# Optimization experiments

Measured on AMD Instinct MI355X. Metric: run time of the kernel, lower is better.

The kernel has to match this reference:

```python
import jax, jax.numpy as jnp
import numpy as np

B, N, C, K = 8, 49104, 90, 1000  # batch, anchors, classes, pre-NMS top-k cap
NEG = -1e9


def _decode(reg, anc):
    # anchors ltrb -> cxcywh, apply reg, back to ltrb (matches decode_boxes)
    l, t, r, b = anc[..., 0], anc[..., 1], anc[..., 2], anc[..., 3]
    w_a, h_a = r - l, b - t
    cx_a, cy_a = l + w_a / 2, t + h_a / 2
    cx = cx_a + reg[..., 0] * w_a
    cy = cy_a + reg[..., 1] * h_a
    w = w_a * jnp.exp(reg[..., 2])
    h = h_a * jnp.exp(reg[..., 3])
    left, top = cx - w / 2, cy - h / 2
    return jnp.stack([left, top, left + w, top + h], -1)


def _iou(boxes):  # [K,4] -> [K,K]
    area = (boxes[:, 2] - boxes[:, 0]) * (boxes[:, 3] - boxes[:, 1])
    lt = jnp.maximum(boxes[:, None, :2], boxes[None, :, :2])
    rb = jnp.minimum(boxes[:, None, 2:], boxes[None, :, 2:])
    wh = jnp.clip(rb - lt, 0.0)
    inter = wh[..., 0] * wh[..., 1]
    return inter / (area[:, None] + area[None, :] - inter + 1e-9)


def _per_image(cls, reg, anchors, size, size_ori, score_thresh, nms_thresh):
    scores = jnp.max(cls, axis=-1)                       # [N]
    labels = jnp.argmax(cls, axis=-1).astype(jnp.int32)  # [N]
    valid = scores >= score_thresh
    boxes = _decode(reg, anchors)                        # [N,4] ltrb
    H = size[0].astype(jnp.float32)
    W = size[1].astype(jnp.float32)
    x = jnp.clip(boxes[..., 0::2], 0.0, W - 1.0)
    y = jnp.clip(boxes[..., 1::2], 0.0, H - 1.0)
    boxes = jnp.stack([x[..., 0], y[..., 0], x[..., 1], y[..., 1]], -1)
    # fixed-size substitute for nonzero(): take top-K by masked score
    ms = jnp.where(valid, scores, NEG)
    top_s, idx = jax.lax.top_k(ms, K)
    b, l, v = boxes[idx], labels[idx], valid[idx]        # [K,4],[K],[K]
    # batched_nms trick: offset boxes per class so classes never overlap
    off = l.astype(jnp.float32) * (jnp.maximum(W, H) + 1.0)
    iou = _iou(b + off[:, None])                         # [K,K]
    ar = jnp.arange(K)
    def body(i, supp):
        keep_i = v[i] & jnp.logical_not(supp[i])
        return supp | (keep_i & (iou[i] > nms_thresh) & (ar > i))
    supp = jax.lax.fori_loop(0, K, body, jnp.zeros((K,), bool))
    keep = v & jnp.logical_not(supp)
    scale = size_ori[0].astype(jnp.float32) / H
    b = b * scale
    out5 = jnp.concatenate(
        [jnp.where(keep[:, None], b, 0.0), jnp.where(keep, top_s, 0.0)[:, None]], -1)
    return out5, jnp.where(keep, l, -1), keep


def setup_inputs() -> dict:
    key = jax.random.key(0)
    k1, k2, k3, k4, k5, k6 = jax.random.split(key, 6)
    classifications = jax.random.uniform(k1, (B, N, C), dtype=jnp.float32)
    regressions = jax.random.normal(k2, (B, N, 4), dtype=jnp.float32) * 0.1
    cx = jax.random.uniform(k3, (N,), minval=0.0, maxval=512.0)
    cy = jax.random.uniform(k4, (N,), minval=0.0, maxval=512.0)
    w = jax.random.uniform(k5, (N,), minval=16.0, maxval=256.0)
    h = jax.random.uniform(k6, (N,), minval=16.0, maxval=256.0)
    anchors = jnp.stack([cx - w / 2, cy - h / 2, cx + w / 2, cy + h / 2], -1)
    return {
        'classifications': classifications,
        'regressions': regressions,
        'anchors': anchors,
        'image_sizes': jnp.full((B, 2), 512, dtype=jnp.int32),
        'image_sizes_ori': jnp.full((B, 2), 768, dtype=jnp.int32),
        'score_thresh': jnp.float32(0.999),
        'nms_thresh': jnp.float32(0.5),
    }


def reference(classifications, regressions, anchors, image_sizes, image_sizes_ori, score_thresh, nms_thresh):
    out5, labels, keep = jax.vmap(
        _per_image, in_axes=(0, 0, None, 0, 0, None, None))(
        classifications, regressions, anchors, image_sizes, image_sizes_ori,
        score_thresh, nms_thresh)
    return out5, labels, keep
```

## Files before the change

kernel.cpp:

```cpp
#include <hip/hip_runtime.h>
#include <stdint.h>

#define NB 8
#define NN 49104
#define NNP 49152
#define NC 90
#define NK 1000
#define CAP2 8192
#define SEG 1024
#define CHUNK 6144
#define NB2 4352
#define NB2P 5120

typedef unsigned long long u64;

__global__ void k_score(const float* __restrict__ cls,
                        const float* __restrict__ thr_p,
                        u64* __restrict__ keys) {
  __shared__ float lds[64 * NC];
  int b = blockIdx.y;
  int t0 = blockIdx.x * 64;
  int acnt = NN - t0; if (acnt > 64) acnt = 64;
  const float4* src = (const float4*)(cls + ((size_t)b * NN + t0) * NC);
  float4* dst = (float4*)lds;
  int elems4 = acnt * NC / 4;
  for (int t = threadIdx.x; t < elems4; t += 256) dst[t] = src[t];
  __syncthreads();
  int a = threadIdx.x >> 2, q = threadIdx.x & 3;
  float best = -1e30f; int bc = 0;
  if (a < acnt) {
    for (int c = q; c < NC; c += 4) {
      float v = lds[a * NC + c];
      if (v > best) { best = v; bc = c; }
    }
    float ov; int oc;
    ov = __shfl_xor(best, 1); oc = __shfl_xor(bc, 1);
    if (ov > best || (ov == best && oc < bc)) { best = ov; bc = oc; }
    ov = __shfl_xor(best, 2); oc = __shfl_xor(bc, 2);
    if (ov > best || (ov == best && oc < bc)) { best = ov; bc = oc; }
  }
  if (q == 0) {
    unsigned idx = (unsigned)(t0 + a);
    u64 key = 0ULL;
    if (a < acnt && best >= *thr_p)
      key = ((u64)__float_as_uint(best) << 32) |
            ((u64)(0xFFFFu - idx) << 16) | (u64)(unsigned)bc;
    keys[(size_t)b * NNP + idx] = key;
  }
}

__global__ __launch_bounds__(1024) void k_compact(const u64* __restrict__ keys,
                                                  u64* __restrict__ ckeys,
                                                  unsigned* __restrict__ segcnt) {
  __shared__ unsigned scnt;
  int tid = threadIdx.x;
  int lane = tid & 63;
  int b = blockIdx.y, chunk = blockIdx.x;
  if (tid == 0) scnt = 0u;
  __syncthreads();
  const u64* src = keys + (size_t)b * NNP + (size_t)chunk * CHUNK;
  u64* dst = ckeys + (size_t)b * CAP2 + (size_t)chunk * SEG;
  u64 k0 = src[tid], k1 = src[tid + 1024], k2 = src[tid + 2048];
  u64 k3 = src[tid + 3072], k4 = src[tid + 4096], k5 = src[tid + 5120];
  u64 lmask = (1ULL << lane) - 1ULL;
  u64 kk[6] = {k0, k1, k2, k3, k4, k5};
#pragma unroll
  for (int j = 0; j < 6; j++) {
    u64 key = kk[j];
    bool valid = key != 0ULL;
    u64 m = __ballot(valid);
    if (m) {
      int leader = (int)__ffsll((unsigned long long)m) - 1;
      unsigned base = 0;
      if (lane == leader) base = atomicAdd(&scnt, (unsigned)__popcll(m));
      base = __shfl(base, leader);
      if (valid) {
        unsigned pos = base + (unsigned)__popcll(m & lmask);
        if (pos < SEG) dst[pos] = key;
      }
    }
  }
  __syncthreads();
  if (tid == 0) {
    unsigned total = scnt; if (total > SEG) total = SEG;
    segcnt[b * 8 + chunk] = total;
  }
}

__device__ __forceinline__ void decode_box(const float4 rg, const float4 an,
                                           float W, float H, float* out) {
#pragma clang fp contract(off)
  float l = an.x, t = an.y, r = an.z, bo = an.w;
  float wa = r - l, ha = bo - t;
  float cxa = l + wa * 0.5f, cya = t + ha * 0.5f;
  float cx = cxa + rg.x * wa;
  float cy = cya + rg.y * ha;
  float w = wa * expf(rg.z);
  float h = ha * expf(rg.w);
  float left = cx - w * 0.5f, top = cy - h * 0.5f;
  float right = left + w, botm = top + h;
  out[0] = fminf(fmaxf(left, 0.f), W - 1.f);
  out[1] = fminf(fmaxf(top, 0.f), H - 1.f);
  out[2] = fminf(fmaxf(right, 0.f), W - 1.f);
  out[3] = fminf(fmaxf(botm, 0.f), H - 1.f);
}

__global__ __launch_bounds__(1024) void k_worker(
    const u64* __restrict__ ckeys, const unsigned* __restrict__ segcnt,
    const float* __restrict__ regs, const float* __restrict__ anch,
    const int* __restrict__ isz, const int* __restrict__ iszo,
    const float* __restrict__ nthr_p, float* __restrict__ out) {
#pragma clang fp contract(off)
  __shared__ __align__(16) char S[151552];
  __shared__ unsigned wsum[16];
  __shared__ unsigned sofs[9];
  __shared__ int lcnt[NC];
  __shared__ int lofs[NC + 1];

  u64* cand = (u64*)S;
  u64* outk = (u64*)(S + 65536);
  unsigned* hist = (unsigned*)(S + 131072);

  int tid = threadIdx.x;
  int lane = tid & 63, wid = tid >> 6;
  int b = blockIdx.x;

  for (int i = tid; i < NB2P; i += 1024) hist[i] = 0u;
  if (tid == 0) {
    unsigned acc = 0;
    for (int s = 0; s < 8; s++) {
      unsigned c = segcnt[b * 8 + s]; if (c > SEG) c = SEG;
      sofs[s] = acc; acc += c;
    }
    sofs[8] = acc;
  }
  __syncthreads();
  unsigned total = sofs[8];

  for (int s = 0; s < 8; s++) {
    unsigned o = sofs[s], c = sofs[s + 1] - o;
    const u64* srcp = ckeys + (size_t)b * CAP2 + (size_t)s * SEG;
    for (unsigned i = tid; i < c; i += 1024) cand[o + i] = srcp[i];
  }
  __syncthreads();

  for (unsigned p = tid; p < total; p += 1024) {
    unsigned bin = (0x3F800000u - (unsigned)(cand[p] >> 32) - 1u) >> 2;
    if (bin >= NB2) bin = NB2 - 1;
    atomicAdd(&hist[bin], 1u);
  }
  __syncthreads();

  int base5 = tid * 5;
  unsigned mysum = 0;
#pragma unroll
  for (int i = 0; i < 5; i++) mysum += hist[base5 + i];
  unsigned v = mysum;
  for (int d = 1; d < 64; d <<= 1) {
    unsigned o = __shfl_up(v, d);
    if (lane >= d) v += o;
  }
  if (lane == 63) wsum[wid] = v;
  __syncthreads();
  if (tid == 0) {
    unsigned acc = 0;
    for (int w2 = 0; w2 < 16; w2++) { unsigned c = wsum[w2]; wsum[w2] = acc; acc += c; }
  }
  __syncthreads();
  unsigned running = wsum[wid] + v - mysum;
#pragma unroll
  for (int i = 0; i < 5; i++) {
    unsigned c = hist[base5 + i];
    hist[base5 + i] = running;
    running += c;
  }
  __syncthreads();

  for (unsigned p = tid; p < total; p += 1024) {
    u64 key = cand[p];
    unsigned bin = (0x3F800000u - (unsigned)(key >> 32) - 1u) >> 2;
    if (bin >= NB2) bin = NB2 - 1;
    unsigned pos = atomicAdd(&hist[bin], 1u);
    if (pos < CAP2) outk[pos] = key;
  }
  __syncthreads();

  for (int bin = tid; bin < NB2; bin += 1024) {
    unsigned hi = hist[bin];
    unsigned lo = bin ? hist[bin - 1] : 0u;
    if (hi > CAP2) hi = CAP2;
    if (lo > CAP2) lo = CAP2;
    if (hi > lo + 1) {
      for (unsigned i2 = lo + 1; i2 < hi; i2++) {
        u64 kx = outk[i2];
        int j = (int)i2 - 1;
        while (j >= (int)lo && outk[j] < kx) { outk[j + 1] = outk[j]; j--; }
        outk[j + 1] = kx;
      }
    }
  }
  __syncthreads();

  int n = (int)total; if (n > NK) n = NK;
  float4* bo = (float4*)S;
  unsigned short* llab = (unsigned short*)(S + 16000);
  unsigned short* sidx = (unsigned short*)(S + 18000);
  unsigned char* live = (unsigned char*)(S + 20000);
  u64* clsbits = (u64*)(S + 21008);
  u64* nmsmask = (u64*)(S + 32536);

  float H = (float)isz[b * 2 + 0];
  float W = (float)isz[b * 2 + 1];
  float scale = (float)iszo[b * 2 + 0] / H;
  float offmul = fmaxf(W, H) + 1.0f;
  for (int i = tid; i < NC * 16; i += 1024) clsbits[i] = 0ULL;
  for (int k = tid; k < n; k += 1024) {
    u64 key = outk[k];
    float sc = __uint_as_float((unsigned)(key >> 32));
    unsigned idx = 0xFFFFu - (unsigned)((key >> 16) & 0xFFFFull);
    int lab = (int)(key & 0xFFFFull);
    float raw[4];
    float4 rg = ((const float4*)regs)[(size_t)b * NN + idx];
    float4 an = ((const float4*)anch)[idx];
    decode_box(rg, an, W, H, raw);
    float off = (float)lab * offmul;
    bo[k] = make_float4(raw[0] + off, raw[1] + off, raw[2] + off, raw[3] + off);
    llab[k] = (unsigned short)lab;
    live[k] = 1;
    int g = b * NK + k;
    float* o5 = out + (size_t)g * 5;
    o5[0] = raw[0] * scale; o5[1] = raw[1] * scale;
    o5[2] = raw[2] * scale; o5[3] = raw[3] * scale;
    o5[4] = sc;
    out[(size_t)NB * NK * 5 + g] = (float)lab;
  }
  __syncthreads();

  for (int k = tid; k < n; k += 1024)
    atomicOr(&clsbits[(int)llab[k] * 16 + (k >> 6)], 1ULL << (k & 63));
  __syncthreads();

  if (tid < NC) {
    unsigned cnt = 0;
#pragma unroll
    for (int w = 0; w < 16; w++) cnt += (unsigned)__popcll(clsbits[tid * 16 + w]);
    lcnt[tid] = (int)cnt;
  }
  __syncthreads();
  if (tid == 0) {
    int acc = 0;
    for (int c = 0; c < NC; c++) { lofs[c] = acc; acc += lcnt[c]; }
    lofs[NC] = acc;
  }
  __syncthreads();

  for (int k = tid; k < n; k += 1024) {
    int lab = (int)llab[k];
    const u64* cb = &clsbits[lab * 16];
    int w0 = k >> 6;
    unsigned pos = 0;
    for (int w = 0; w < w0; w++) pos += (unsigned)__popcll(cb[w]);
    pos += (unsigned)__popcll(cb[w0] & ((1ULL << (k & 63)) - 1ULL));
    sidx[lofs[lab] + pos] = (unsigned short)k;
  }
  __syncthreads();

  float thr = *nthr_p;
  for (int p = tid; p < n; p += 1024) {
    int ki = (int)sidx[p];
    int lab = (int)llab[ki];
    int s = lofs[lab], e = lofs[lab + 1];
    int r = p - s;
    if (r < 64) {
      u64 mask = 0ULL;
      float4 Bb = bo[ki];
      float x0 = Bb.x, y0 = Bb.y, x1 = Bb.z, y1 = Bb.w;
      float ai = (x1 - x0) * (y1 - y0);
      int qe = e; if (qe > s + 64) qe = s + 64;
      for (int q = p + 1; q < qe; q++) {
        int kj = (int)sidx[q];
        float4 Cc = bo[kj];
        float aj = (Cc.z - Cc.x) * (Cc.w - Cc.y);
        float ltx = fmaxf(x0, Cc.x), lty = fmaxf(y0, Cc.y);
        float rbx = fminf(x1, Cc.z), rby = fminf(y1, Cc.w);
        float ww = fmaxf(rbx - ltx, 0.f), hh = fmaxf(rby - lty, 0.f);
        float inter = ww * hh;
        float den = ((ai + aj) - inter) + 1e-9f;
        float iou = inter / den;
        if (iou > thr) mask |= 1ULL << (q - s);
      }
      nmsmask[lab * 64 + r] = mask;
    }
  }
  __syncthreads();

  if (tid < NC) {
    int s = lofs[tid], e = lofs[tid + 1], m = e - s;
    if (m <= 64) {
      u64 rem = 0ULL;
      for (int r = 0; r < m; r++)
        if (!((rem >> r) & 1ULL)) rem |= nmsmask[tid * 64 + r];
      for (int r = 0; r < m; r++)
        live[(int)sidx[s + r]] = (unsigned char)(1ULL ^ ((rem >> r) & 1ULL));
    } else {
      for (int r = 0; r < m; r++) live[(int)sidx[s + r]] = 1;
      for (int i = s; i < e; i++) {
        int ki = (int)sidx[i];
        if (!live[ki]) continue;
        float4 Bb = bo[ki];
        float x0 = Bb.x, y0 = Bb.y, x1 = Bb.z, y1 = Bb.w;
        float ai = (x1 - x0) * (y1 - y0);
        for (int j = i + 1; j < e; j++) {
          int kj = (int)sidx[j];
          if (!live[kj]) continue;
          float4 Cc = bo[kj];
          float aj = (Cc.z - Cc.x) * (Cc.w - Cc.y);
          float ltx = fmaxf(x0, Cc.x), lty = fmaxf(y0, Cc.y);
          float rbx = fminf(x1, Cc.z), rby = fminf(y1, Cc.w);
          float ww = fmaxf(rbx - ltx, 0.f), hh = fmaxf(rby - lty, 0.f);
          float inter = ww * hh;
          float den = ((ai + aj) - inter) + 1e-9f;
          float iou = inter / den;
          if (iou > thr) live[kj] = 0;
        }
      }
    }
  }
  __syncthreads();

  for (int k = tid; k < NK; k += 1024) {
    int g = b * NK + k;
    int keep = (k < n) ? (int)live[k] : 0;
    if (keep) {
      out[(size_t)NB * NK * 6 + g] = 1.0f;
    } else {
      float* o5 = out + (size_t)g * 5;
      o5[0] = 0.f; o5[1] = 0.f; o5[2] = 0.f; o5[3] = 0.f; o5[4] = 0.f;
      out[(size_t)NB * NK * 5 + g] = -1.0f;
      out[(size_t)NB * NK * 6 + g] = 0.0f;
    }
  }
}

extern "C" void kernel_launch(void* const* d_in, const int* in_sizes, int n_in,
                              void* d_out, int out_size, void* d_ws, size_t ws_size,
                              hipStream_t stream) {
  const float* cls = (const float*)d_in[0];
  const float* regs = (const float*)d_in[1];
  const float* anch = (const float*)d_in[2];
  const int* isz = (const int*)d_in[3];
  const int* iszo = (const int*)d_in[4];
  const float* sthr = (const float*)d_in[5];
  const float* nthr = (const float*)d_in[6];
  float* out = (float*)d_out;

  char* p = (char*)d_ws;
  auto alloc = [&](size_t bytes) {
    char* r = p;
    p += (bytes + 255) & ~(size_t)255;
    return r;
  };
  u64* keys = (u64*)alloc((size_t)NB * NNP * 8);
  u64* ckeys = (u64*)alloc((size_t)NB * CAP2 * 8);
  unsigned* segcnt = (unsigned*)alloc((size_t)NB * 8 * 4);

  hipLaunchKernelGGL(k_score, dim3(NNP / 64, NB), dim3(256), 0, stream,
                     cls, sthr, keys);
  hipLaunchKernelGGL(k_compact, dim3(8, NB), dim3(1024), 0, stream,
                     keys, ckeys, segcnt);
  hipLaunchKernelGGL(k_worker, dim3(NB), dim3(1024), 0, stream,
                     ckeys, segcnt, regs, anch, isz, iszo, nthr, out);
}
```

Baseline: 58.43 us.

## Fuse compaction into score kernel with per-block segments and in-worker prefix scan

The score kernel now handles 192 anchors per block and compacts above-threshold keys in shared memory using ballot and atomics. It writes them straight to per-block segments with a count, so the separate compaction kernel and the dense key array are gone. The worker kernel prefix-scans 256 segment counts and fuses the gather with histogram building. This removes one launch and a full-size key write and read, at the cost of larger score blocks (768 threads, about 69KB of shared memory) and more, smaller segments to gather in the worker.

```diff
diff --git a/kernel.cpp b/kernel.cpp
--- a/kernel.cpp
+++ b/kernel.cpp
@@ -3,30 +3,35 @@
 
 #define NB 8
 #define NN 49104
-#define NNP 49152
 #define NC 90
 #define NK 1000
+#define SA 192
+#define NSEG 256
 #define CAP2 8192
-#define SEG 1024
-#define CHUNK 6144
 #define NB2 4352
 #define NB2P 5120
 
 typedef unsigned long long u64;
 
-__global__ void k_score(const float* __restrict__ cls,
-                        const float* __restrict__ thr_p,
-                        u64* __restrict__ keys) {
-  __shared__ float lds[64 * NC];
+__global__ __launch_bounds__(768) void k_score(const float* __restrict__ cls,
+                                               const float* __restrict__ thr_p,
+                                               u64* __restrict__ cseg,
+                                               unsigned* __restrict__ segcnt) {
+  __shared__ __align__(16) float lds[SA * NC];
+  __shared__ unsigned scnt;
   int b = blockIdx.y;
-  int t0 = blockIdx.x * 64;
-  int acnt = NN - t0; if (acnt > 64) acnt = 64;
+  int blk = blockIdx.x;
+  int t0 = blk * SA;
+  int tid = threadIdx.x;
+  int lane = tid & 63;
+  if (tid == 0) scnt = 0u;
+  int acnt = NN - t0; if (acnt > SA) acnt = SA;
   const float4* src = (const float4*)(cls + ((size_t)b * NN + t0) * NC);
   float4* dst = (float4*)lds;
   int elems4 = acnt * NC / 4;
-  for (int t = threadIdx.x; t < elems4; t += 256) dst[t] = src[t];
-  __syncthreads();
-  int a = threadIdx.x >> 2, q = threadIdx.x & 3;
+  for (int t = tid; t < elems4; t += 768) dst[t] = src[t];
+  __syncthreads();
+  int a = tid >> 2, q = tid & 3;
   float best = -1e30f; int bc = 0;
   if (a < acnt) {
     for (int c = q; c < NC; c += 4) {
@@ -39,52 +44,31 @@
     ov = __shfl_xor(best, 2); oc = __shfl_xor(bc, 2);
     if (ov > best || (ov == best && oc < bc)) { best = ov; bc = oc; }
   }
-  if (q == 0) {
+  bool valid = (q == 0) && (a < acnt) && (best >= *thr_p);
+  u64 key = 0ULL;
+  if (valid) {
     unsigned idx = (unsigned)(t0 + a);
-    u64 key = 0ULL;
-    if (a < acnt && best >= *thr_p)
-      key = ((u64)__float_as_uint(best) << 32) |
-            ((u64)(0xFFFFu - idx) << 16) | (u64)(unsigned)bc;
-    keys[(size_t)b * NNP + idx] = key;
-  }
-}
-
-__global__ __launch_bounds__(1024) void k_compact(const u64* __restrict__ keys,
-                                                  u64* __restrict__ ckeys,
-                                                  unsigned* __restrict__ segcnt) {
-  __shared__ unsigned scnt;
-  int tid = threadIdx.x;
-  int lane = tid & 63;
-  int b = blockIdx.y, chunk = blockIdx.x;
-  if (tid == 0) scnt = 0u;
-  __syncthreads();
-  const u64* src = keys + (size_t)b * NNP + (size_t)chunk * CHUNK;
-  u64* dst = ckeys + (size_t)b * CAP2 + (size_t)chunk * SEG;
-  u64 k0 = src[tid], k1 = src[tid + 1024], k2 = src[tid + 2048];
-  u64 k3 = src[tid + 3072], k4 = src[tid + 4096], k5 = src[tid + 5120];
-  u64 lmask = (1ULL << lane) - 1ULL;
-  u64 kk[6] = {k0, k1, k2, k3, k4, k5};
-#pragma unroll
-  for (int j = 0; j < 6; j++) {
-    u64 key = kk[j];
-    bool valid = key != 0ULL;
-    u64 m = __ballot(valid);
-    if (m) {
-      int leader = (int)__ffsll((unsigned long long)m) - 1;
-      unsigned base = 0;
-      if (lane == leader) base = atomicAdd(&scnt, (unsigned)__popcll(m));
-      base = __shfl(base, leader);
-      if (valid) {
-        unsigned pos = base + (unsigned)__popcll(m & lmask);
-        if (pos < SEG) dst[pos] = key;
-      }
-    }
-  }
-  __syncthreads();
-  if (tid == 0) {
-    unsigned total = scnt; if (total > SEG) total = SEG;
-    segcnt[b * 8 + chunk] = total;
-  }
+    key = ((u64)__float_as_uint(best) << 32) |
+          ((u64)(0xFFFFu - idx) << 16) | (u64)(unsigned)bc;
+  }
+  __syncthreads();
+  u64* kbuf = (u64*)lds;
+  u64 m = __ballot(valid);
+  if (m) {
+    int leader = (int)__ffsll((unsigned long long)m) - 1;
+    unsigned base = 0;
+    if (lane == leader) base = atomicAdd(&scnt, (unsigned)__popcll(m));
+    base = __shfl(base, leader);
+    if (valid) {
+      unsigned pos = base + (unsigned)__popcll(m & ((1ULL << lane) - 1ULL));
+      kbuf[pos] = key;
+    }
+  }
+  __syncthreads();
+  unsigned cnt = scnt;
+  u64* dseg = cseg + ((size_t)b * NSEG + blk) * SA;
+  for (unsigned t = tid; t < cnt; t += 768) dseg[t] = kbuf[t];
+  if (tid == 0) segcnt[b * NSEG + blk] = cnt;
 }
 
 __device__ __forceinline__ void decode_box(const float4 rg, const float4 an,
@@ -106,14 +90,16 @@
 }
 
 __global__ __launch_bounds__(1024) void k_worker(
-    const u64* __restrict__ ckeys, const unsigned* __restrict__ segcnt,
+    const u64* __restrict__ cseg, const unsigned* __restrict__ segcnt,
     const float* __restrict__ regs, const float* __restrict__ anch,
     const int* __restrict__ isz, const int* __restrict__ iszo,
     const float* __restrict__ nthr_p, float* __restrict__ out) {
 #pragma clang fp contract(off)
   __shared__ __align__(16) char S[151552];
   __shared__ unsigned wsum[16];
-  __shared__ unsigned sofs[9];
+  __shared__ unsigned segc[NSEG];
+  __shared__ unsigned sofsL[NSEG + 1];
+  __shared__ unsigned wcar[4];
   __shared__ int lcnt[NC];
   __shared__ int lofs[NC + 1];
 
@@ -126,28 +112,45 @@
   int b = blockIdx.x;
 
   for (int i = tid; i < NB2P; i += 1024) hist[i] = 0u;
-  if (tid == 0) {
-    unsigned acc = 0;
-    for (int s = 0; s < 8; s++) {
-      unsigned c = segcnt[b * 8 + s]; if (c > SEG) c = SEG;
-      sofs[s] = acc; acc += c;
-    }
-    sofs[8] = acc;
-  }
-  __syncthreads();
-  unsigned total = sofs[8];
-
-  for (int s = 0; s < 8; s++) {
-    unsigned o = sofs[s], c = sofs[s + 1] - o;
-    const u64* srcp = ckeys + (size_t)b * CAP2 + (size_t)s * SEG;
-    for (unsigned i = tid; i < c; i += 1024) cand[o + i] = srcp[i];
-  }
-  __syncthreads();
-
-  for (unsigned p = tid; p < total; p += 1024) {
-    unsigned bin = (0x3F800000u - (unsigned)(cand[p] >> 32) - 1u) >> 2;
-    if (bin >= NB2) bin = NB2 - 1;
-    atomicAdd(&hist[bin], 1u);
+  if (tid < NSEG) {
+    unsigned c = segcnt[b * NSEG + tid]; if (c > SA) c = SA;
+    segc[tid] = c;
+  }
+  __syncthreads();
+
+  unsigned vv = 0;
+  if (tid < NSEG) {
+    vv = segc[tid];
+    for (int d = 1; d < 64; d <<= 1) {
+      unsigned o = __shfl_up(vv, d);
+      if (lane >= d) vv += o;
+    }
+    if (lane == 63) wcar[wid] = vv;
+  }
+  __syncthreads();
+  if (tid < NSEG) {
+    unsigned add = 0;
+    for (int w = 0; w < wid; w++) add += wcar[w];
+    sofsL[tid] = add + vv - segc[tid];
+    if (tid == NSEG - 1) sofsL[NSEG] = add + vv;
+  }
+  __syncthreads();
+  unsigned total = sofsL[NSEG]; if (total > CAP2) total = CAP2;
+
+  {
+    int s = tid >> 2, sub = tid & 3;
+    unsigned c = segc[s], o = sofsL[s];
+    const u64* srcp = cseg + ((size_t)b * NSEG + s) * SA;
+    for (unsigned j = sub; j < c; j += 4) {
+      u64 key = srcp[j];
+      unsigned pos = o + j;
+      if (pos < CAP2) {
+        cand[pos] = key;
+        unsigned bin = (0x3F800000u - (unsigned)(key >> 32) - 1u) >> 2;
+        if (bin >= NB2) bin = NB2 - 1;
+        atomicAdd(&hist[bin], 1u);
+      }
+    }
   }
   __syncthreads();
 
@@ -360,14 +363,11 @@
     p += (bytes + 255) & ~(size_t)255;
     return r;
   };
-  u64* keys = (u64*)alloc((size_t)NB * NNP * 8);
-  u64* ckeys = (u64*)alloc((size_t)NB * CAP2 * 8);
-  unsigned* segcnt = (unsigned*)alloc((size_t)NB * 8 * 4);
-
-  hipLaunchKernelGGL(k_score, dim3(NNP / 64, NB), dim3(256), 0, stream,
-                     cls, sthr, keys);
-  hipLaunchKernelGGL(k_compact, dim3(8, NB), dim3(1024), 0, stream,
-                     keys, ckeys, segcnt);
+  u64* cseg = (u64*)alloc((size_t)NB * NSEG * SA * 8);
+  unsigned* segcnt = (unsigned*)alloc((size_t)NB * NSEG * 4);
+
+  hipLaunchKernelGGL(k_score, dim3(NSEG, NB), dim3(768), 0, stream,
+                     cls, sthr, cseg, segcnt);
   hipLaunchKernelGGL(k_worker, dim3(NB), dim3(1024), 0, stream,
-                     ckeys, segcnt, regs, anch, isz, iszo, nthr, out);
+                     cseg, segcnt, regs, anch, isz, iszo, nthr, out);
 }
```

Measured after the change: 55.59 us. -4.9%, faster.
